# Optimization experiments

Hardware: AMD Instinct MI355X
Metric: run time of the kernel (lower is better)

## Reference

```python
import jax, jax.numpy as jnp
import numpy as np
import math

N = 100000      # nodes
E = 500000      # edges
IN = 128        # in_dim
QD = 64         # quantum_dim
FEAT = 2 * QD   # entanglement layer input dim (real+imag concat)
OUT = 128       # out_dim
H = 4           # num_heads
HD = OUT // H   # head_dim
NQ = 8          # num_qubits


def _lin(x, w, b):
    # torch nn.Linear: y = x @ W^T + b, W has shape [out, in]
    return x @ w.T + b


def _layernorm(x, g, b, eps=1e-5):
    m = x.mean(-1, keepdims=True)
    v = x.var(-1, keepdims=True)
    return (x - m) * jax.lax.rsqrt(v + eps) * g + b


def setup_inputs() -> dict:
    key = jax.random.key(0)
    ks = jax.random.split(key, 26)
    rn = lambda k, shape, s=0.05: (jax.random.normal(k, shape, jnp.float32) * s)
    inp = {
        "x": jax.random.normal(ks[0], (N, IN), jnp.float32),
        "edge_index": jax.random.randint(ks[1], (2, E), 0, N, jnp.int64),
        # QuantumStateEmbedding params
        "sp_w": rn(ks[2], (2 * QD, IN)), "sp_b": rn(ks[3], (2 * QD,)),
        "ln1_g": jnp.ones((2 * QD,), jnp.float32), "ln1_b": jnp.zeros((2 * QD,), jnp.float32),
        "phase_gates": jax.random.normal(ks[4], (NQ, QD), jnp.float32),
        "amp_w": rn(ks[5], (QD, QD)), "amp_b": rn(ks[6], (QD,)),
        "ph_w": rn(ks[7], (QD, QD)), "ph_b": rn(ks[8], (QD,)),
        # QuantumEntanglementLayer params
        "ent_w": rn(ks[9], (2 * OUT, 2 * FEAT)), "ent_b": rn(ks[10], (2 * OUT,)),
        "q_w": rn(ks[11], (OUT, FEAT)), "q_b": rn(ks[12], (OUT,)),
        "k_w": rn(ks[13], (OUT, FEAT)), "k_b": rn(ks[14], (OUT,)),
        "v_w": rn(ks[15], (OUT, FEAT)), "v_b": rn(ks[16], (OUT,)),
        "meas_w": rn(ks[17], (4, OUT, OUT)), "meas_b": rn(ks[18], (4, OUT)),
        "out_w": rn(ks[19], (OUT, OUT)), "out_b": rn(ks[20], (OUT,)),
        # final LayerNorm
        "ln2_g": jnp.ones((OUT,), jnp.float32), "ln2_b": jnp.zeros((OUT,), jnp.float32),
    }
    return inp


def reference(x, edge_index, sp_w, sp_b, ln1_g, ln1_b, phase_gates, amp_w, amp_b,
              ph_w, ph_b, ent_w, ent_b, q_w, q_b, k_w, k_b, v_w, v_b,
              meas_w, meas_b, out_w, out_b, ln2_g, ln2_b):
    # --- QuantumStateEmbedding ---
    qs = jnp.tanh(_layernorm(_lin(x, sp_w, sp_b), ln1_g, ln1_b))  # [N, 2QD]
    real, imag = qs[:, :QD], qs[:, QD:]
    # sum over qubit axis of phase_gates * real  ==  real * phase_gates.sum(0)
    pm = real * phase_gates.sum(0)
    amp = jax.nn.sigmoid(_lin(real, amp_w, amp_b))
    ph = jnp.tanh(_lin(imag, ph_w, ph_b)) * math.pi
    ang = ph + pm
    qf = jnp.concatenate([amp * jnp.cos(ang), amp * jnp.sin(ang)], axis=-1)  # [N, FEAT]

    # --- QuantumEntanglementLayer (PyG: x_i = target, x_j = source, aggr='add') ---
    src, tgt = edge_index[0], edge_index[1]
    x_i = qf[tgt]   # [E, FEAT]
    x_j = qf[src]
    ent = _lin(jnp.concatenate([x_i, x_j], axis=-1), ent_w, ent_b)  # [E, 2*OUT]
    ei, ej = ent[:, :OUT], ent[:, OUT:]
    q = _lin(x_i, q_w, q_b).reshape(E, H, HD)
    k = _lin(x_j, k_w, k_b).reshape(E, H, HD)
    v = _lin(x_j, v_w, v_b).reshape(E, H, HD)
    scores = (q * k).sum(-1, keepdims=True) / math.sqrt(HD)  # [E, H, 1]
    w = jax.nn.softmax(scores, axis=1)                       # softmax over heads (as in source)
    qm = (w * v).reshape(E, OUT)
    # 4 measurement ops: op(ei)*op(ej), then mean over ops
    mi = jnp.einsum('ei,koi->eko', ei, meas_w) + meas_b[None]  # [E, 4, OUT]
    mj = jnp.einsum('ei,koi->eko', ej, meas_w) + meas_b[None]
    measured = (mi * mj).mean(axis=1)                          # [E, OUT]
    msg = _lin(qm + measured, out_w, out_b)
    agg = jax.ops.segment_sum(msg, tgt, num_segments=N)        # scatter-add aggregate

    # --- norm + GELU (torch nn.GELU default = exact) ---
    return jax.nn.gelu(_layernorm(agg, ln2_g, ln2_b), approximate=False)
```

## Files before the change

kernel.cpp:

```cpp
#include <hip/hip_runtime.h>
#include <math.h>

#define NN 100000
#define EE 500000
#define NNB  1563
#define NFB2 1563
#define NWB  25000

typedef __attribute__((ext_vector_type(8))) short short8;
typedef __attribute__((ext_vector_type(4))) float f32x4;
#define Z4 (f32x4){0,0,0,0}

#define C16(row, ch) (((row)<<4) + ((ch) ^ ((row)&7)))
#define E16(row, col) ((C16((row),(col)>>3)<<3) + ((col)&7))

__device__ __forceinline__ f32x4 mfma16(short8 a, short8 b, f32x4 c){
    return __builtin_amdgcn_mfma_f32_16x16x32_bf16(a, b, c, 0, 0, 0);
}
__device__ __forceinline__ short f2bf(float f){
    union { float f; unsigned u; } v; v.f = f;
    unsigned r = v.u + 0x7fffu + ((v.u >> 16) & 1u);
    return (short)(r >> 16);
}
__device__ __forceinline__ float bf2f(short s){
    union { unsigned u; float f; } v; v.u = ((unsigned)(unsigned short)s) << 16;
    return v.f;
}
__device__ __forceinline__ short8 bfrag(const short* __restrict__ W, int K, int ct, int ks, int lane){
    return *(const short8*)(W + (long)(ct*16 + (lane&15))*K + ks*32 + (lane>>4)*8);
}
__device__ __forceinline__ int fragmap(int o, int k){
    return (((o>>4)*4 + (k>>5))*64 + (((k>>3)&3)*16 + (o&15)))*8 + (k&7);
}

__global__ __launch_bounds__(256) void prep_kernel(
    const float* __restrict__ q_w, const float* __restrict__ k_w,
    const float* __restrict__ v_w, const float* __restrict__ out_w,
    const float* __restrict__ sp_w, const float* __restrict__ amp_w,
    const float* __restrict__ ph_w, short* __restrict__ dst)
{
    int i = blockIdx.x*256 + threadIdx.x;
    if (i >= 90112) return;
    float v; int base = -1, loc = 0;
    if      (i < 16384){ v = q_w[i];         base = 0;     loc = i; }
    else if (i < 32768){ v = k_w[i-16384];   base = 16384; loc = i-16384; }
    else if (i < 49152){ v = v_w[i-32768];   base = 32768; loc = i-32768; }
    else if (i < 65536){ v = out_w[i-49152]; base = 49152; loc = i-49152; }
    else if (i < 81920) v = sp_w[i-65536];
    else if (i < 86016) v = amp_w[i-81920];
    else                v = ph_w[i-86016];
    if (base >= 0) dst[base + fragmap(loc>>7, loc&127)] = f2bf(v);
    else           dst[i] = f2bf(v);
}

__global__ __launch_bounds__(256) void combine_kernel(
    const float* __restrict__ ent_w, const float* __restrict__ meas_w,
    short* __restrict__ wCi, short* __restrict__ wCj)
{
    const int b = blockIdx.x;
    const int kk = b >> 7, half = (b >> 6) & 1, ot = (b >> 3) & 7, ct = b & 7;
    const int tid = threadIdx.x;
    const int o = ot*16 + (tid >> 4);
    const int c = ct*32 + (tid & 15)*2;
    const float* mrow  = meas_w + ((long)(kk*128 + o) << 7);
    const float* wbase = ent_w + (long)(half*128)*256 + c;
    float a0 = 0.f, a1 = 0.f;
    #pragma unroll 8
    for (int k = 0; k < 128; k++){
        float m = mrow[k];
        float2 wv = *(const float2*)(wbase + (long)k*256);
        a0 = fmaf(m, wv.x, a0);
        a1 = fmaf(m, wv.y, a1);
    }
    const int ct_o = o>>4, l15o = o&15;
    const int halfc = c>>7, cr = c&127;
    const int ksn = cr>>5, lhn = (cr>>3)&3, iin = cr&7;
    const long idx = ((((long)(kk*8 + ct_o)*2 + halfc)*4 + ksn)*64 + (lhn*16 + l15o))*8 + iin;
    short* dst = (half ? wCj : wCi) + idx;
    dst[0] = f2bf(a0); dst[1] = f2bf(a1);
}
__global__ __launch_bounds__(256) void combine_bias_kernel(
    const float* __restrict__ meas_w, const float* __restrict__ ent_b,
    const float* __restrict__ meas_b,
    float* __restrict__ bci, float* __restrict__ bcj)
{
    int id = blockIdx.x*256 + threadIdx.x;
    int kk = id >> 8, half = (id >> 7) & 1, o = id & 127;
    const float* mrow = meas_w + ((long)(kk*128 + o) << 7);
    const float* eb = ent_b + half*128;
    float a = meas_b[kk*128 + o];
    #pragma unroll 8
    for (int k = 0; k < 128; k++) a = fmaf(mrow[k], eb[k], a);
    (half ? bcj : bci)[kk*128 + o] = a;
}

__global__ __launch_bounds__(256) void hist_kernel(const int* __restrict__ eidx, int* __restrict__ hist){
    int i = blockIdx.x*256 + threadIdx.x;
    if (i < EE) atomicAdd(&hist[eidx[EE+i]], 1);
}
__global__ __launch_bounds__(512) void scanA_kernel(const int* __restrict__ hist,
                                                    int* __restrict__ scanv, int* __restrict__ bsum){
    __shared__ int s[512];
    const int tid = threadIdx.x;
    const int i = blockIdx.x*512 + tid;
    int v = hist[i];
    s[tid] = v;
    __syncthreads();
    #pragma unroll
    for (int d=1; d<512; d<<=1){
        int t = (tid>=d) ? s[tid-d] : 0;
        __syncthreads();
        s[tid] += t;
        __syncthreads();
    }
    scanv[i] = s[tid] - v;
    if (tid==511) bsum[blockIdx.x] = s[511];
}
__global__ __launch_bounds__(256) void scanB_kernel(const int* __restrict__ bsum, int* __restrict__ boff){
    __shared__ int s[256];
    const int tid = threadIdx.x;
    int v = (tid<196) ? bsum[tid] : 0;
    s[tid] = v;
    __syncthreads();
    #pragma unroll
    for (int d=1; d<256; d<<=1){
        int t = (tid>=d) ? s[tid-d] : 0;
        __syncthreads();
        s[tid] += t;
        __syncthreads();
    }
    if (tid<196) boff[tid] = s[tid] - v;
}
__global__ __launch_bounds__(256) void scatter_kernel(const int* __restrict__ eidx,
    const int* __restrict__ scanv, const int* __restrict__ boff, int* __restrict__ cnt,
    int* __restrict__ sSrc)
{
    int i = blockIdx.x*256 + threadIdx.x;
    if (i >= EE) return;
    int t = eidx[EE+i], sv = eidx[i];
    int r = atomicAdd(&cnt[t], 1);
    int pos = scanv[t] + boff[t>>9] + r;
    sSrc[pos] = sv;
}

__global__ __launch_bounds__(512) void node_kernel(
    const float* __restrict__ x,
    const short* __restrict__ wSP, const float* __restrict__ sp_b,
    const float* __restrict__ ln1_g, const float* __restrict__ ln1_b,
    const float* __restrict__ pg,
    const short* __restrict__ wA, const float* __restrict__ amp_b,
    const short* __restrict__ wP, const float* __restrict__ ph_b,
    short* __restrict__ qfb)
{
    __shared__ short xb[64*128];
    __shared__ float yb[64*132];
    __shared__ short qsb[64*128];
    __shared__ float pgs[64];

    const int tid = threadIdx.x;
    const int lane = tid & 63;
    const int w    = tid >> 6;
    const int l15  = lane & 15;
    const int lj   = (lane >> 4) << 2;
    const int n0   = blockIdx.x * 64;

    if (tid < 64){
        float s = 0.f;
        #pragma unroll
        for (int r=0;r<8;r++) s += pg[r*64 + tid];
        pgs[tid] = s;
    }
    for (int t = tid; t < 1024; t += 512){
        int e = t >> 4, c8 = t & 15;
        int n = n0 + e; if (n >= NN) n = NN-1;
        const float4* xg = (const float4*)(x + (long)n*128 + c8*8);
        float4 a = xg[0], b = xg[1];
        short8 sv;
        sv[0]=f2bf(a.x); sv[1]=f2bf(a.y); sv[2]=f2bf(a.z); sv[3]=f2bf(a.w);
        sv[4]=f2bf(b.x); sv[5]=f2bf(b.y); sv[6]=f2bf(b.z); sv[7]=f2bf(b.w);
        ((short8*)xb)[C16(e, c8)] = sv;
    }
    __syncthreads();

    const short8* xbv = (const short8*)xb;
    const int col = (w<<4) + l15;

    {
        f32x4 acc[4];
        #pragma unroll
        for (int r=0;r<4;r++) acc[r]=Z4;
        #pragma unroll
        for (int ks=0; ks<4; ks++){
            short8 bw = bfrag(wSP,128,w,ks,lane);
            #pragma unroll
            for (int r=0;r<4;r++){
                int row = r*16+l15;
                acc[r] = mfma16(xbv[(row<<4) + (((ks<<2)+(lane>>4)) ^ (row&7))], bw, acc[r]);
            }
        }
        float bias = sp_b[col];
        #pragma unroll
        for (int r=0;r<4;r++){
            #pragma unroll
            for (int j=0;j<4;j++)
                yb[(r*16+lj+j)*132 + col] = acc[r][j] + bias;
        }
    }
    __syncthreads();

    {
        const int row = tid >> 3, cs = tid & 7;
        float v[16];
        float s = 0.f, sq = 0.f;
        #pragma unroll
        for (int i=0;i<16;i++){
            v[i] = yb[row*132 + cs*16 + i];
            s += v[i]; sq += v[i]*v[i];
        }
        #pragma unroll
        for (int m=1;m<8;m<<=1){ s += __shfl_xor(s,m); sq += __shfl_xor(sq,m); }
        float mean = s*(1.0f/128.0f);
        float rstd = rsqrtf(sq*(1.0f/128.0f) - mean*mean + 1e-5f);
        short8 s0, s1;
        #pragma unroll
        for (int i=0;i<16;i++){
            int c = cs*16 + i;
            float q = tanhf((v[i]-mean)*rstd*ln1_g[c] + ln1_b[c]);
            if (i<8) s0[i] = f2bf(q); else s1[i-8] = f2bf(q);
        }
        ((short8*)qsb)[C16(row, cs*2  )] = s0;
        ((short8*)qsb)[C16(row, cs*2+1)] = s1;
    }
    __syncthreads();

    {
        const short8* qv = (const short8*)qsb;
        const int isPh = w >> 2;
        const int ct   = w & 3;
        f32x4 a4[4];
        #pragma unroll
        for (int r=0;r<4;r++) a4[r]=Z4;
        #pragma unroll
        for (int ks=0; ks<2; ks++){
            short8 bw = bfrag(isPh ? wP : wA, 64, ct, ks, lane);
            #pragma unroll
            for (int r=0;r<4;r++){
                int row = r*16+l15;
                int ch = isPh*8 + (ks<<2)+(lane>>4);
                a4[r] = mfma16(qv[(row<<4) + (ch ^ (row&7))], bw, a4[r]);
            }
        }
        const int oc = ct*16 + l15;
        float bs = isPh ? ph_b[oc] : amp_b[oc];
        #pragma unroll
        for (int r=0;r<4;r++){
            #pragma unroll
            for (int j=0;j<4;j++){
                float vv = a4[r][j] + bs;
                float ov = isPh ? tanhf(vv)*3.14159265358979323846f
                                : 1.0f/(1.0f+expf(-vv));
                yb[(r*16+lj+j)*132 + isPh*64 + oc] = ov;
            }
        }
    }
    __syncthreads();

    {
        const int row = tid >> 3, cs = tid & 7;
        const int n = n0 + row;
        short8 outc, outs;
        #pragma unroll
        for (int i=0;i<8;i++){
            int c = cs*8 + i;
            float amp  = yb[row*132 + c];
            float ph   = yb[row*132 + 64 + c];
            float real = bf2f(qsb[E16(row, c)]);
            float ang  = ph + real*pgs[c];
            outc[i] = f2bf(amp * cosf(ang));
            outs[i] = f2bf(amp * sinf(ang));
        }
        if (n < NN){
            *(short8*)(qfb + (long)n*128 + cs*8)      = outc;
            *(short8*)(qfb + (long)n*128 + 64 + cs*8) = outs;
        }
    }
}

__global__ __launch_bounds__(512) void qkvpb_kernel(
    const short* __restrict__ qfb,
    const short* __restrict__ wK, const float* __restrict__ k_b,
    const short* __restrict__ wV, const float* __restrict__ v_b,
    const short* __restrict__ wQ, const float* __restrict__ q_b,
    const short* __restrict__ wCi, const short* __restrict__ wCj,
    short* __restrict__ knvp)
{
    __shared__ short a1[64*128];
    const int tid=threadIdx.x, lane=tid&63, w=tid>>6;
    const int l15=lane&15, lh=lane>>4, lj=lh<<2;
    const long n0=(long)blockIdx.x*64;
    for (int t=tid;t<1024;t+=512){
        int e=t>>4,c8=t&15;
        ((short8*)a1)[C16(e,c8)] = ((const short8*)(qfb+(n0+e)*128))[c8];
    }
    __syncthreads();
    short8 A[4][4];
    #pragma unroll
    for (int rt=0;rt<4;rt++)
        #pragma unroll
        for (int ks=0;ks<4;ks++)
            A[rt][ks] = ((const short8*)a1)[C16(rt*16+l15, (ks<<2)+lh)];
    const int col = (w<<4)+l15;

    {
        f32x4 acc[4];
        #pragma unroll
        for (int rt=0;rt<4;rt++) acc[rt]=Z4;
        #pragma unroll
        for (int ks=0;ks<4;ks++){
            short8 b = *(const short8*)(wK + ((w*4+ks)*64 + lane)*8);
            #pragma unroll
            for (int rt=0;rt<4;rt++) acc[rt]=mfma16(A[rt][ks],b,acc[rt]);
        }
        float bias=k_b[col];
        #pragma unroll
        for (int rt=0;rt<4;rt++)
            #pragma unroll
            for (int j=0;j<4;j++)
                knvp[(n0+rt*16+lj+j)*512 + col]=f2bf(acc[rt][j]+bias);
    }
    {
        f32x4 acc[4];
        #pragma unroll
        for (int rt=0;rt<4;rt++) acc[rt]=Z4;
        #pragma unroll
        for (int ks=0;ks<4;ks++){
            short8 b = *(const short8*)(wV + ((w*4+ks)*64 + lane)*8);
            #pragma unroll
            for (int rt=0;rt<4;rt++) acc[rt]=mfma16(A[rt][ks],b,acc[rt]);
        }
        float bias=v_b[col];
        #pragma unroll
        for (int rt=0;rt<4;rt++)
            #pragma unroll
            for (int j=0;j<4;j++)
                knvp[(n0+rt*16+lj+j)*512 + 128 + col]=f2bf(acc[rt][j]+bias);
    }
    {
        f32x4 acc[4];
        #pragma unroll
        for (int rt=0;rt<4;rt++) acc[rt]=Z4;
        #pragma unroll
        for (int ks=0;ks<4;ks++){
            short8 b = *(const short8*)(wQ + ((w*4+ks)*64 + lane)*8);
            #pragma unroll
            for (int rt=0;rt<4;rt++) acc[rt]=mfma16(A[rt][ks],b,acc[rt]);
        }
        float bias=q_b[col];
        #pragma unroll
        for (int rt=0;rt<4;rt++)
            #pragma unroll
            for (int j=0;j<4;j++)
                knvp[(n0+rt*16+lj+j)*512 + 384 + col]=f2bf(acc[rt][j]+bias);
    }
    {
        f32x4 pbacc[4];
        #pragma unroll
        for (int rt=0;rt<4;rt++) pbacc[rt]=Z4;
        #pragma unroll 1
        for (int kk=0;kk<4;kk++){
            short8 bi[4], bj[4];
            #pragma unroll
            for (int ks=0;ks<4;ks++){
                long fi = (((long)(kk*8 + w)*2 + 1)*4 + ks)*512 + lane*8;
                bi[ks] = *(const short8*)(wCi + fi);
                bj[ks] = *(const short8*)(wCj + fi);
            }
            #pragma unroll
            for (int rt=0;rt<4;rt++){
                f32x4 ai=Z4, aj=Z4;
                #pragma unroll
                for (int ks=0;ks<4;ks++){
                    ai = mfma16(A[rt][ks], bi[ks], ai);
                    aj = mfma16(A[rt][ks], bj[ks], aj);
                }
                #pragma unroll
                for (int j=0;j<4;j++) pbacc[rt][j] += ai[j]*aj[j];
            }
        }
        #pragma unroll
        for (int rt=0;rt<4;rt++)
            #pragma unroll
            for (int j=0;j<4;j++)
                knvp[(n0+rt*16+lj+j)*512 + 256 + col]=f2bf(pbacc[rt][j]);
    }
}

__global__ __launch_bounds__(256) void walk_kernel(
    const short* __restrict__ qfb, short* __restrict__ knvp,
    const int* __restrict__ sSrc, const int* __restrict__ hist,
    const int* __restrict__ scanv, const int* __restrict__ boff,
    short* __restrict__ aqmpb)
{
    const int tid=threadIdx.x, lane=tid&63, w=tid>>6;
    const int n = blockIdx.x*4 + w;
    const int g = lane >> 4;
    const int cl = (lane & 15) * 8;
    const float sc = 0.17677669529663688f;

    const int rp0 = scanv[n] + boff[n>>9];
    const int dg  = hist[n];

    float q8[8];
    {
        short8 qv = *(const short8*)(knvp + (long)n*512 + 384 + cl);
        #pragma unroll
        for (int i=0;i<8;i++) q8[i]=bf2f(qv[i]);
    }
    float aq[8], s[8], p[8];
    #pragma unroll
    for (int i=0;i<8;i++){ aq[i]=0.f; s[i]=0.f; p[i]=0.f; }

    bool vCur = (g < dg);
    int  sCur = vCur ? sSrc[rp0+g] : 0;
    const short* bCur = knvp + (long)sCur*512;
    short8 k8 = *(const short8*)(bCur + cl);
    short8 v8 = *(const short8*)(bCur + 128 + cl);
    short8 p8 = *(const short8*)(bCur + 256 + cl);
    short8 f8 = *(const short8*)(qfb + (long)sCur*128 + cl);

    #pragma unroll 1
    for (int e=0; e<dg; e+=4){
        const int en = e + 4 + g;
        const bool vN = (en < dg);
        const int  sN = vN ? sSrc[rp0+en] : 0;
        const short* bN = knvp + (long)sN*512;
        short8 kN = *(const short8*)(bN + cl);
        short8 vN8= *(const short8*)(bN + 128 + cl);
        short8 pN = *(const short8*)(bN + 256 + cl);
        short8 fN = *(const short8*)(qfb + (long)sN*128 + cl);

        float d = 0.f;
        #pragma unroll
        for (int i=0;i<8;i++) d += q8[i]*bf2f(k8[i]);
        d += __shfl_xor(d,1); d += __shfl_xor(d,2);
        d *= sc;
        float mx = fmaxf(d, __shfl_xor(d,4));
        mx = fmaxf(mx, __shfl_xor(mx,8));
        float eh = expf(d - mx);
        float den = eh;
        den += __shfl_xor(den,4); den += __shfl_xor(den,8);
        float wgt = vCur ? (eh/den) : 0.f;
        float mv  = vCur ? 1.f : 0.f;
        #pragma unroll
        for (int i=0;i<8;i++){
            aq[i] += wgt * bf2f(v8[i]);
            s[i]  += mv  * bf2f(f8[i]);
            p[i]  += mv  * bf2f(p8[i]);
        }
        k8=kN; v8=vN8; p8=pN; f8=fN; vCur=vN;
    }
    #pragma unroll
    for (int i=0;i<8;i++){
        aq[i] += __shfl_xor(aq[i],16); aq[i] += __shfl_xor(aq[i],32);
        s[i]  += __shfl_xor(s[i],16);  s[i]  += __shfl_xor(s[i],32);
        p[i]  += __shfl_xor(p[i],16);  p[i]  += __shfl_xor(p[i],32);
    }
    if (lane < 16){
        short8 av, pv, sv;
        #pragma unroll
        for (int i=0;i<8;i++){ av[i]=f2bf(aq[i]); pv[i]=f2bf(p[i]); sv[i]=f2bf(s[i]); }
        *(short8*)(aqmpb + (long)n*256 + cl)       = av;
        *(short8*)(aqmpb + (long)n*256 + 128 + cl) = pv;
        *(short8*)(knvp  + (long)n*512 + 384 + cl) = sv;
    }
}

__global__ __launch_bounds__(256) void final_kernel(
    const short* __restrict__ qfb, const short* __restrict__ knvp,
    const int* __restrict__ hist,
    const short* __restrict__ wCi, const short* __restrict__ wCj,
    const float* __restrict__ bci, const float* __restrict__ bcj,
    const short* __restrict__ wO, const float* __restrict__ out_b,
    const float* __restrict__ g2, const float* __restrict__ b2,
    const short* __restrict__ aqmpb, float* __restrict__ outp)
{
    __shared__ __align__(16) char smem[32768];
    __shared__ int degs[64];
    short* a1   = (short*)smem;
    short* Sbf  = (short*)(smem + 16384);
    short* ybh  = (short*)(smem + 16384);

    const int tid=threadIdx.x, lane=tid&63, w=tid>>6;
    const int l15=lane&15, lh=lane>>4, lj=lh<<2;
    const long n0=(long)blockIdx.x*64;

    if (tid < 64) degs[tid] = hist[n0+tid];
    for (int t=tid;t<1024;t+=256){
        int e=t>>4,c8=t&15;
        long n = n0+e; if (n >= NN) n = NN-1;
        ((short8*)a1)[C16(e,c8)]  = ((const short8*)(qfb+n*128))[c8];
        ((short8*)Sbf)[C16(e,c8)] = *(const short8*)(knvp + n*512 + 384 + c8*8);
    }
    __syncthreads();

    const short8* a1v = (const short8*)a1;
    const short8* sfv = (const short8*)Sbf;
    const int col0 = (2*w)*16 + l15;
    const int col1 = (2*w+1)*16 + l15;

    f32x4 tt[2][4], cr[2][4];
    #pragma unroll
    for (int ci=0;ci<2;ci++)
        #pragma unroll
        for (int rt=0;rt<4;rt++){ tt[ci][rt]=Z4; cr[ci][rt]=Z4; }

    #pragma unroll 1
    for (int kk=0; kk<4; kk++){
        #pragma unroll
        for (int ci=0; ci<2; ci++){
            const int ctt = 2*w + ci;
            const int col = ci ? col1 : col0;
            const long fb = (long)(kk*8 + ctt)*8;
            short8 Pa[4], Pj[4];
            #pragma unroll
            for (int ks=0;ks<4;ks++){
                Pa[ks] = *(const short8*)(wCi + (fb + ks)*512 + lane*8);
                Pj[ks] = *(const short8*)(wCj + (fb + ks)*512 + lane*8);
            }
            f32x4 aiA[4], ajA[4];
            #pragma unroll
            for (int rt=0;rt<4;rt++){
                f32x4 ai=Z4, aj=Z4;
                #pragma unroll
                for (int ks=0;ks<4;ks++){
                    short8 fq = a1v[C16(rt*16+l15,(ks<<2)+lh)];
                    ai = mfma16(fq, Pa[ks], ai);
                    aj = mfma16(fq, Pj[ks], aj);
                }
                aiA[rt]=ai; ajA[rt]=aj;
            }
            short8 Qa[4], Qj[4];
            #pragma unroll
            for (int ks=0;ks<4;ks++){
                Qa[ks] = *(const short8*)(wCi + (fb + 4 + ks)*512 + lane*8);
                Qj[ks] = *(const short8*)(wCj + (fb + 4 + ks)*512 + lane*8);
            }
            float ci_=bci[kk*128+col], cj_=bcj[kk*128+col];
            #pragma unroll
            for (int rt=0;rt<4;rt++){
                f32x4 sbi=Z4, sbj=Z4;
                #pragma unroll
                for (int ks=0;ks<4;ks++){
                    short8 fs = sfv[C16(rt*16+l15,(ks<<2)+lh)];
                    sbi = mfma16(fs, Qa[ks], sbi);
                    sbj = mfma16(fs, Qj[ks], sbj);
                }
                #pragma unroll
                for (int j=0;j<4;j++){
                    float AI = aiA[rt][j]+ci_, AJ = ajA[rt][j]+cj_;
                    tt[ci][rt][j] += AI*AJ;
                    cr[ci][rt][j] += AI*sbj[j] + sbi[j]*AJ;
                }
            }
        }
    }
    __syncthreads();

    short* msgb = a1;
    #pragma unroll
    for (int ci=0;ci<2;ci++){
        const int col = ci ? col1 : col0;
        #pragma unroll
        for (int rt=0;rt<4;rt++){
            #pragma unroll
            for (int j=0;j<4;j++){
                int row = rt*16+lj+j;
                long nc = n0+row; if (nc >= NN) nc = NN-1;
                float ms = bf2f(aqmpb[nc*256 + col])
                         + 0.25f*((float)degs[row]*tt[ci][rt][j] + cr[ci][rt][j]
                                  + bf2f(aqmpb[nc*256 + 128 + col]));
                msgb[(C16(row, col>>3)<<3) + (col&7)] = f2bf(ms);
            }
        }
    }
    __syncthreads();

    const short8* mbv = (const short8*)msgb;
    #pragma unroll
    for (int ci=0; ci<2; ci++){
        const int ctt = 2*w + ci;
        const int col = ci ? col1 : col0;
        short8 bo[4];
        #pragma unroll
        for (int ks=0;ks<4;ks++)
            bo[ks] = *(const short8*)(wO + ((long)(ctt*4+ks))*512 + lane*8);
        float ob = out_b[col];
        #pragma unroll
        for (int rt=0;rt<4;rt++){
            f32x4 ao=Z4;
            #pragma unroll
            for (int ks=0;ks<4;ks++)
                ao = mfma16(mbv[C16(rt*16+l15,(ks<<2)+lh)], bo[ks], ao);
            #pragma unroll
            for (int j=0;j<4;j++){
                int row = rt*16+lj+j;
                ybh[(C16(row, col>>3)<<3) + (col&7)] = f2bf(ao[j] + (float)degs[row]*ob);
            }
        }
    }
    __syncthreads();

    const short8* ybv = (const short8*)ybh;
    #pragma unroll
    for (int half=0; half<2; half++){
        const int row = half*32 + (tid>>3), cs = tid&7;
        const long n = n0+row;
        float v[16]; float sum=0.f, sq=0.f;
        {
            short8 c0 = ybv[C16(row, cs*2)];
            short8 c1 = ybv[C16(row, cs*2+1)];
            #pragma unroll
            for (int i=0;i<8;i++){ v[i]   = bf2f(c0[i]); }
            #pragma unroll
            for (int i=0;i<8;i++){ v[8+i] = bf2f(c1[i]); }
        }
        #pragma unroll
        for (int i=0;i<16;i++){ sum+=v[i]; sq+=v[i]*v[i]; }
        #pragma unroll
        for (int m=1;m<8;m<<=1){ sum+=__shfl_xor(sum,m); sq+=__shfl_xor(sq,m); }
        float mean=sum*(1.0f/128.0f);
        float rstd=rsqrtf(sq*(1.0f/128.0f)-mean*mean+1e-5f);
        if (n < NN){
            float o[16];
            #pragma unroll
            for (int i=0;i<16;i++){
                int c=cs*16+i;
                float y=(v[i]-mean)*rstd*g2[c]+b2[c];
                o[i]=0.5f*y*(1.0f+erff(y*0.70710678118f));
            }
            float* dst = outp + n*128 + cs*16;
            #pragma unroll
            for (int i=0;i<4;i++)
                ((float4*)dst)[i] = (float4){o[i*4],o[i*4+1],o[i*4+2],o[i*4+3]};
        }
    }
}

extern "C" void kernel_launch(void* const* d_in, const int* in_sizes, int n_in,
                              void* d_out, int out_size, void* d_ws, size_t ws_size,
                              hipStream_t stream)
{
    const float* x      = (const float*)d_in[0];
    const int*   eidx   = (const int*)  d_in[1];
    const float* sp_w   = (const float*)d_in[2];
    const float* sp_b   = (const float*)d_in[3];
    const float* ln1_g  = (const float*)d_in[4];
    const float* ln1_b  = (const float*)d_in[5];
    const float* pg     = (const float*)d_in[6];
    const float* amp_w  = (const float*)d_in[7];
    const float* amp_b  = (const float*)d_in[8];
    const float* ph_w   = (const float*)d_in[9];
    const float* ph_b   = (const float*)d_in[10];
    const float* ent_w  = (const float*)d_in[11];
    const float* ent_b  = (const float*)d_in[12];
    const float* q_w    = (const float*)d_in[13];
    const float* q_b    = (const float*)d_in[14];
    const float* k_w    = (const float*)d_in[15];
    const float* k_b    = (const float*)d_in[16];
    const float* v_w    = (const float*)d_in[17];
    const float* v_b    = (const float*)d_in[18];
    const float* meas_w = (const float*)d_in[19];
    const float* meas_b = (const float*)d_in[20];
    const float* out_w  = (const float*)d_in[21];
    const float* out_b  = (const float*)d_in[22];
    const float* ln2_g  = (const float*)d_in[23];
    const float* ln2_b  = (const float*)d_in[24];

    char* wsb = (char*)d_ws;
    short* qfb  = (short*)(wsb + 0);
    short* knvp = (short*)(wsb + 25608192);
    short* wAll = (short*)(wsb + 128040960);
    short* wCi  = (short*)(wsb + 128221184);
    short* wCj  = (short*)(wsb + 128483328);
    float* bci  = (float*)(wsb + 128745472);
    float* bcj  = (float*)(wsb + 128747520);
    int* hist   = (int*)(wsb + 128749568);
    int* cnt    = (int*)(wsb + 129150976);
    int* scanv  = (int*)(wsb + 129552384);
    int* bsum   = (int*)(wsb + 129953792);
    int* boff   = (int*)(wsb + 129954816);
    int* sSrc   = (int*)(wsb + 129955840);

    if (ws_size < 132000000ull) return;

    short* wQ  = wAll;
    short* wK  = wAll + 16384;
    short* wV  = wAll + 32768;
    short* wO  = wAll + 49152;
    short* wSP = wAll + 65536;
    short* wA  = wAll + 81920;
    short* wP  = wAll + 86016;

    short* aqmpb = (short*)d_out;

    hipMemsetAsync(hist, 0, 401408, stream);
    hipMemsetAsync(cnt,  0, 401408, stream);

    prep_kernel<<<352, 256, 0, stream>>>(q_w, k_w, v_w, out_w, sp_w, amp_w, ph_w, wAll);
    combine_kernel<<<512, 256, 0, stream>>>(ent_w, meas_w, wCi, wCj);
    combine_bias_kernel<<<4, 256, 0, stream>>>(meas_w, ent_b, meas_b, bci, bcj);
    node_kernel<<<NNB, 512, 0, stream>>>(x, wSP, sp_b, ln1_g, ln1_b, pg,
                                         wA, amp_b, wP, ph_b, qfb);
    hist_kernel<<<(EE+255)/256, 256, 0, stream>>>(eidx, hist);
    scanA_kernel<<<196, 512, 0, stream>>>(hist, scanv, bsum);
    scanB_kernel<<<1, 256, 0, stream>>>(bsum, boff);
    scatter_kernel<<<(EE+255)/256, 256, 0, stream>>>(eidx, scanv, boff, cnt, sSrc);
    qkvpb_kernel<<<NNB, 512, 0, stream>>>(qfb, wK, k_b, wV, v_b, wQ, q_b,
                                          wCi, wCj, knvp);
    walk_kernel<<<NWB, 256, 0, stream>>>(qfb, knvp, sSrc, hist, scanv, boff, aqmpb);
    final_kernel<<<NFB2, 256, 0, stream>>>(qfb, knvp, hist,
                                           wCi, wCj, bci, bcj, wO, out_b,
                                           ln2_g, ln2_b, aqmpb, (float*)d_out);
}
```

Before: 443.2 us.

## Retile final kernel to 128 nodes per block with 8 waves

The final kernel now handles 128 nodes per block with 512 threads. Each of the 8 waves owns one 16-column tile across 8 row tiles, where before 4 waves each owned two column tiles across 4 row tiles. Each wave's combined-weight fragments are loaded once per kk and reused over twice as many rows, which halves global weight traffic per node. The cost is 64KB of shared memory per block and more accumulator registers, which may lower occupancy.

```diff
diff --git a/kernel.cpp b/kernel.cpp
--- a/kernel.cpp
+++ b/kernel.cpp
@@ -4,7 +4,7 @@
 #define NN 100000
 #define EE 500000
 #define NNB  1563
-#define NFB2 1563
+#define NFB3 782
 #define NWB  25000
 
 typedef __attribute__((ext_vector_type(8))) short short8;
@@ -475,7 +475,7 @@
     }
 }
 
-__global__ __launch_bounds__(256) void final_kernel(
+__global__ __launch_bounds__(512) void final_kernel(
     const short* __restrict__ qfb, const short* __restrict__ knvp,
     const int* __restrict__ hist,
     const short* __restrict__ wCi, const short* __restrict__ wCj,
@@ -484,18 +484,18 @@
     const float* __restrict__ g2, const float* __restrict__ b2,
     const short* __restrict__ aqmpb, float* __restrict__ outp)
 {
-    __shared__ __align__(16) char smem[32768];
-    __shared__ int degs[64];
+    __shared__ __align__(16) char smem[65536];
+    __shared__ int degs[128];
     short* a1   = (short*)smem;
-    short* Sbf  = (short*)(smem + 16384);
-    short* ybh  = (short*)(smem + 16384);
+    short* Sbf  = (short*)(smem + 32768);
+    short* ybh  = (short*)(smem + 32768);
 
     const int tid=threadIdx.x, lane=tid&63, w=tid>>6;
     const int l15=lane&15, lh=lane>>4, lj=lh<<2;
-    const long n0=(long)blockIdx.x*64;
-
-    if (tid < 64) degs[tid] = hist[n0+tid];
-    for (int t=tid;t<1024;t+=256){
+    const long n0=(long)blockIdx.x*128;
+
+    if (tid < 128) degs[tid] = hist[n0+tid];
+    for (int t=tid;t<2048;t+=512){
         int e=t>>4,c8=t&15;
         long n = n0+e; if (n >= NN) n = NN-1;
         ((short8*)a1)[C16(e,c8)]  = ((const short8*)(qfb+n*128))[c8];
@@ -505,62 +505,41 @@
 
     const short8* a1v = (const short8*)a1;
     const short8* sfv = (const short8*)Sbf;
-    const int col0 = (2*w)*16 + l15;
-    const int col1 = (2*w+1)*16 + l15;
-
-    f32x4 tt[2][4], cr[2][4];
-    #pragma unroll
-    for (int ci=0;ci<2;ci++)
-        #pragma unroll
-        for (int rt=0;rt<4;rt++){ tt[ci][rt]=Z4; cr[ci][rt]=Z4; }
+    const int col = (w<<4) + l15;
+
+    f32x4 tt[8], cr[8];
+    #pragma unroll
+    for (int rt=0;rt<8;rt++){ tt[rt]=Z4; cr[rt]=Z4; }
 
     #pragma unroll 1
     for (int kk=0; kk<4; kk++){
-        #pragma unroll
-        for (int ci=0; ci<2; ci++){
-            const int ctt = 2*w + ci;
-            const int col = ci ? col1 : col0;
-            const long fb = (long)(kk*8 + ctt)*8;
-            short8 Pa[4], Pj[4];
+        const long fb = (long)(kk*8 + w)*8;
+        short8 Pa[4], Pj[4], Qa[4], Qj[4];
+        #pragma unroll
+        for (int ks=0;ks<4;ks++){
+            Pa[ks] = *(const short8*)(wCi + (fb + ks)*512 + lane*8);
+            Pj[ks] = *(const short8*)(wCj + (fb + ks)*512 + lane*8);
+            Qa[ks] = *(const short8*)(wCi + (fb + 4 + ks)*512 + lane*8);
+            Qj[ks] = *(const short8*)(wCj + (fb + 4 + ks)*512 + lane*8);
+        }
+        const float ci_=bci[kk*128+col], cj_=bcj[kk*128+col];
+        #pragma unroll
+        for (int rt=0;rt<8;rt++){
+            f32x4 ai=Z4, aj=Z4, sbi=Z4, sbj=Z4;
             #pragma unroll
             for (int ks=0;ks<4;ks++){
-                Pa[ks] = *(const short8*)(wCi + (fb + ks)*512 + lane*8);
-                Pj[ks] = *(const short8*)(wCj + (fb + ks)*512 + lane*8);
-            }
-            f32x4 aiA[4], ajA[4];
-            #pragma unroll
-            for (int rt=0;rt<4;rt++){
-                f32x4 ai=Z4, aj=Z4;
-                #pragma unroll
-                for (int ks=0;ks<4;ks++){
-                    short8 fq = a1v[C16(rt*16+l15,(ks<<2)+lh)];
-                    ai = mfma16(fq, Pa[ks], ai);
-                    aj = mfma16(fq, Pj[ks], aj);
-                }
-                aiA[rt]=ai; ajA[rt]=aj;
-            }
-            short8 Qa[4], Qj[4];
-            #pragma unroll
-            for (int ks=0;ks<4;ks++){
-                Qa[ks] = *(const short8*)(wCi + (fb + 4 + ks)*512 + lane*8);
-                Qj[ks] = *(const short8*)(wCj + (fb + 4 + ks)*512 + lane*8);
-            }
-            float ci_=bci[kk*128+col], cj_=bcj[kk*128+col];
-            #pragma unroll
-            for (int rt=0;rt<4;rt++){
-                f32x4 sbi=Z4, sbj=Z4;
-                #pragma unroll
-                for (int ks=0;ks<4;ks++){
-                    short8 fs = sfv[C16(rt*16+l15,(ks<<2)+lh)];
-                    sbi = mfma16(fs, Qa[ks], sbi);
-                    sbj = mfma16(fs, Qj[ks], sbj);
-                }
-                #pragma unroll
-                for (int j=0;j<4;j++){
-                    float AI = aiA[rt][j]+ci_, AJ = ajA[rt][j]+cj_;
-                    tt[ci][rt][j] += AI*AJ;
-                    cr[ci][rt][j] += AI*sbj[j] + sbi[j]*AJ;
-                }
+                short8 fq = a1v[C16(rt*16+l15,(ks<<2)+lh)];
+                short8 fs = sfv[C16(rt*16+l15,(ks<<2)+lh)];
+                ai  = mfma16(fq, Pa[ks], ai);
+                aj  = mfma16(fq, Pj[ks], aj);
+                sbi = mfma16(fs, Qa[ks], sbi);
+                sbj = mfma16(fs, Qj[ks], sbj);
+            }
+            #pragma unroll
+            for (int j=0;j<4;j++){
+                float AI = ai[j]+ci_, AJ = aj[j]+cj_;
+                tt[rt][j] += AI*AJ;
+                cr[rt][j] += AI*sbj[j] + sbi[j]*AJ;
             }
         }
     }
@@ -568,35 +547,28 @@
 
     short* msgb = a1;
     #pragma unroll
-    for (int ci=0;ci<2;ci++){
-        const int col = ci ? col1 : col0;
-        #pragma unroll
-        for (int rt=0;rt<4;rt++){
-            #pragma unroll
-            for (int j=0;j<4;j++){
-                int row = rt*16+lj+j;
-                long nc = n0+row; if (nc >= NN) nc = NN-1;
-                float ms = bf2f(aqmpb[nc*256 + col])
-                         + 0.25f*((float)degs[row]*tt[ci][rt][j] + cr[ci][rt][j]
-                                  + bf2f(aqmpb[nc*256 + 128 + col]));
-                msgb[(C16(row, col>>3)<<3) + (col&7)] = f2bf(ms);
-            }
+    for (int rt=0;rt<8;rt++){
+        #pragma unroll
+        for (int j=0;j<4;j++){
+            int row = rt*16+lj+j;
+            long nc = n0+row; if (nc >= NN) nc = NN-1;
+            float ms = bf2f(aqmpb[nc*256 + col])
+                     + 0.25f*((float)degs[row]*tt[rt][j] + cr[rt][j]
+                              + bf2f(aqmpb[nc*256 + 128 + col]));
+            msgb[(C16(row, col>>3)<<3) + (col&7)] = f2bf(ms);
         }
     }
     __syncthreads();
 
     const short8* mbv = (const short8*)msgb;
-    #pragma unroll
-    for (int ci=0; ci<2; ci++){
-        const int ctt = 2*w + ci;
-        const int col = ci ? col1 : col0;
+    {
         short8 bo[4];
         #pragma unroll
         for (int ks=0;ks<4;ks++)
-            bo[ks] = *(const short8*)(wO + ((long)(ctt*4+ks))*512 + lane*8);
+            bo[ks] = *(const short8*)(wO + ((long)(w*4+ks))*512 + lane*8);
         float ob = out_b[col];
         #pragma unroll
-        for (int rt=0;rt<4;rt++){
+        for (int rt=0;rt<8;rt++){
             f32x4 ao=Z4;
             #pragma unroll
             for (int ks=0;ks<4;ks++)
@@ -613,7 +585,7 @@
     const short8* ybv = (const short8*)ybh;
     #pragma unroll
     for (int half=0; half<2; half++){
-        const int row = half*32 + (tid>>3), cs = tid&7;
+        const int row = half*64 + (tid>>3), cs = tid&7;
         const long n = n0+row;
         float v[16]; float sum=0.f, sq=0.f;
         {
@@ -718,7 +690,7 @@
     qkvpb_kernel<<<NNB, 512, 0, stream>>>(qfb, wK, k_b, wV, v_b, wQ, q_b,
                                           wCi, wCj, knvp);
     walk_kernel<<<NWB, 256, 0, stream>>>(qfb, knvp, sSrc, hist, scanv, boff, aqmpb);
-    final_kernel<<<NFB2, 256, 0, stream>>>(qfb, knvp, hist,
+    final_kernel<<<NFB3, 512, 0, stream>>>(qfb, knvp, hist,
                                            wCi, wCj, bci, bcj, wO, out_b,
                                            ln2_g, ln2_b, aqmpb, (float*)d_out);
 }
```

Measured after the change: 621.8 us. 40.3% more time.
